# Performance work log

Measured on AMD Instinct MI355X. Metric: run time of the kernel, lower is better.

Reference implementation:

```python
import jax, jax.numpy as jnp
import numpy as np

IN_FEATURES = 1024
OUT_FEATURES = 1024
NUM_GMM = 5
MAX_STD = 3.0
ROWS = (IN_FEATURES + 1) * OUT_FEATURES  # (in+1)*out rows of GMM params


def setup_inputs() -> dict:
    key = jax.random.key(0)
    kx, km, kl, kw = jax.random.split(key, 4)
    x = jax.random.normal(kx, (4096, IN_FEATURES), dtype=jnp.float32)
    mean = jax.random.normal(km, (ROWS, NUM_GMM), dtype=jnp.float32)
    logstd = jax.random.normal(kl, (ROWS, NUM_GMM), dtype=jnp.float32)
    weight = jax.random.normal(kw, (ROWS, NUM_GMM), dtype=jnp.float32)
    return {"x": x, "mean": mean, "logstd": logstd, "weight": weight}


def reference(x, mean, logstd, weight):
    # GMM weight sampling: Categorical(softmax(weight)) picks a component per row,
    # then Normal(mean_sel, exp(tanh(logstd_sel)*max_std)) is sampled.
    key = jax.random.key(42)
    kcat, knorm = jax.random.split(key)
    # categorical with logits == Categorical(probs=softmax(weight))
    idx = jax.random.categorical(kcat, weight, axis=-1)  # [ROWS] int
    sel_mean = jnp.take_along_axis(mean, idx[:, None], axis=1)[:, 0]      # [ROWS]
    sel_logstd = jnp.take_along_axis(logstd, idx[:, None], axis=1)[:, 0]  # [ROWS]
    sel_std = jnp.exp(jnp.tanh(sel_logstd) * MAX_STD)
    eps = jax.random.normal(knorm, (mean.shape[0],), dtype=mean.dtype)
    weight_bias = sel_mean + sel_std * eps  # torch .sample() -> no grad flow
    weight_bias = jax.lax.stop_gradient(weight_bias)
    bias = weight_bias[:OUT_FEATURES]                                   # [out]
    W = weight_bias[OUT_FEATURES:].reshape(OUT_FEATURES, IN_FEATURES)   # [out, in]
    return x @ W.T + bias
```

## Files before the change

kernel.cpp:

```cpp
#include <hip/hip_runtime.h>
#include <cstdint>
#include <cmath>

#define IN_FEATURES 1024
#define OUT_FEATURES 1024
#define NUM_GMM 5
#define ROWS ((IN_FEATURES + 1) * OUT_FEATURES)

struct U2 { uint32_t a, b; };

__host__ __device__ constexpr uint32_t rotl32c(uint32_t x, int d) {
  return (x << d) | (x >> (32 - d));
}

#define TF_ROUND(r) { x0 += x1; x1 = rotl32c(x1, (r)); x1 ^= x0; }
__host__ __device__ constexpr U2 threefry2x32(uint32_t k0, uint32_t k1,
                                              uint32_t x0, uint32_t x1) {
  const uint32_t ks0 = k0, ks1 = k1, ks2 = k0 ^ k1 ^ 0x1BD11BDAu;
  x0 += ks0; x1 += ks1;
  TF_ROUND(13) TF_ROUND(15) TF_ROUND(26) TF_ROUND(6)
  x0 += ks1; x1 += ks2 + 1u;
  TF_ROUND(17) TF_ROUND(29) TF_ROUND(16) TF_ROUND(24)
  x0 += ks2; x1 += ks0 + 2u;
  TF_ROUND(13) TF_ROUND(15) TF_ROUND(26) TF_ROUND(6)
  x0 += ks0; x1 += ks1 + 3u;
  TF_ROUND(17) TF_ROUND(29) TF_ROUND(16) TF_ROUND(24)
  x0 += ks1; x1 += ks2 + 4u;
  TF_ROUND(13) TF_ROUND(15) TF_ROUND(26) TF_ROUND(6)
  x0 += ks2; x1 += ks0 + 5u;
  return U2{x0, x1};
}

constexpr U2 KC = threefry2x32(0u, 42u, 0u, 0u);
constexpr U2 KN = threefry2x32(0u, 42u, 0u, 1u);
constexpr uint32_t KCAT0  = KC.a;
constexpr uint32_t KCAT1  = KC.b;
constexpr uint32_t KNORM0 = KN.a;
constexpr uint32_t KNORM1 = KN.b;

__device__ inline float u01_from_bits(uint32_t bits) {
  return __uint_as_float((bits >> 9) | 0x3F800000u) - 1.0f;
}

__device__ inline float log_f32_acc(float x) {
  uint32_t ix = __float_as_uint(x);
  int e = (int)(ix >> 23) - 127;
  float mf = __uint_as_float((ix & 0x007FFFFFu) | 0x3F800000u);
  if (mf > 1.4142135381698608f) { mf *= 0.5f; e += 1; }
  double m = (double)mf;
  double d = m + 1.0;
  double r = (double)__builtin_amdgcn_rcpf((float)d);
  r = r * (2.0 - d * r);
  r = r * (2.0 - d * r);
  double t = (m - 1.0) * r;
  double t2 = t * t;
  double p = 1.0 / 15.0;
  p = fma(p, t2, 1.0 / 13.0);
  p = fma(p, t2, 1.0 / 11.0);
  p = fma(p, t2, 1.0 / 9.0);
  p = fma(p, t2, 1.0 / 7.0);
  p = fma(p, t2, 1.0 / 5.0);
  p = fma(p, t2, 1.0 / 3.0);
  p = fma(p, t2, 1.0);
  double res = fma((double)e, 0.693147180559945309417, 2.0 * t * p);
  return (float)res;
}

__device__ inline float u_from_bits_clamped(uint32_t bits) {
  float f = u01_from_bits(bits);
  return fmaxf(1.17549435e-38f, f + 1.17549435e-38f);
}

__device__ inline float gumbel_acc(uint32_t bits) {
  float u = u_from_bits_clamped(bits);
  float t1 = log_f32_acc(u);
  float t2 = log_f32_acc(-t1);
  return -t2;
}

__device__ inline float gumbel_fast(uint32_t bits) {
  float u = u_from_bits_clamped(bits);
  float t1 = __logf(u);
  return -__logf(-t1);
}

__device__ inline float erfinv_xla(float x) {
  float s = (1.0f - x) * (1.0f + x);
  float w = -__logf(s);
  float p;
  if (w < 5.0f) {
    w = w - 2.5f;
    p = 2.81022636e-08f;
    p = fmaf(p, w, 3.43273939e-07f);
    p = fmaf(p, w, -3.5233877e-06f);
    p = fmaf(p, w, -4.39150654e-06f);
    p = fmaf(p, w, 0.00021858087f);
    p = fmaf(p, w, -0.00125372503f);
    p = fmaf(p, w, -0.00417768164f);
    p = fmaf(p, w, 0.246640727f);
    p = fmaf(p, w, 1.50140941f);
  } else {
    w = sqrtf(w) - 3.0f;
    p = -0.000200214257f;
    p = fmaf(p, w, 0.000100950558f);
    p = fmaf(p, w, 0.00134934322f);
    p = fmaf(p, w, -0.00367342844f);
    p = fmaf(p, w, 0.00573950773f);
    p = fmaf(p, w, -0.0076224613f);
    p = fmaf(p, w, 0.00943887047f);
    p = fmaf(p, w, 1.00167406f);
    p = fmaf(p, w, 2.83297682f);
  }
  return p * x;
}

__device__ inline float normal_from_bits(uint32_t bits) {
  float f = u01_from_bits(bits);
  const float lo = -0.99999994f;
  float u = fmaxf(lo, f * 2.0f + lo);
  return 1.4142135623730951f * erfinv_xla(u);
}

__device__ inline unsigned short f32_to_bf16_rne(float f) {
  uint32_t u = __float_as_uint(f);
  return (unsigned short)((u + 0x7FFFu + ((u >> 16) & 1u)) >> 16);
}

__global__ __launch_bounds__(256) void prep_kernel(
    const float* __restrict__ mean, const float* __restrict__ logstd,
    const float* __restrict__ weight, const float* __restrict__ x,
    unsigned short* __restrict__ wh, float* __restrict__ bias_f32,
    unsigned short* __restrict__ xh, int n_chunks) {
  const int r = blockIdx.x * 256 + threadIdx.x;

  const float* wrow = weight + (size_t)r * NUM_GMM;
  const float* mrow = mean   + (size_t)r * NUM_GMM;
  const float* lrow = logstd + (size_t)r * NUM_GMM;
  float wv[NUM_GMM], mv[NUM_GMM], lv[NUM_GMM];
#pragma unroll
  for (int g = 0; g < NUM_GMM; ++g) {
    wv[g] = wrow[g];
    mv[g] = mrow[g];
    lv[g] = lrow[g];
  }

  if (r < n_chunks) {
    int i = r * 8;
    float4 a = *(const float4*)(x + i);
    float4 b = *(const float4*)(x + i + 4);
    union { unsigned short s[8]; uint4 v; } o;
    o.s[0] = f32_to_bf16_rne(a.x); o.s[1] = f32_to_bf16_rne(a.y);
    o.s[2] = f32_to_bf16_rne(a.z); o.s[3] = f32_to_bf16_rne(a.w);
    o.s[4] = f32_to_bf16_rne(b.x); o.s[5] = f32_to_bf16_rne(b.y);
    o.s[6] = f32_to_bf16_rne(b.z); o.s[7] = f32_to_bf16_rne(b.w);
    *(uint4*)(xh + i) = o.v;
  }

  uint32_t bits[NUM_GMM];
  float v[NUM_GMM];
#pragma unroll
  for (int g = 0; g < NUM_GMM; ++g) {
    U2 t = threefry2x32(KCAT0, KCAT1, 0u, (uint32_t)(r * NUM_GMM + g));
    bits[g] = t.a ^ t.b;
    v[g] = gumbel_fast(bits[g]) + wv[g];
  }
  int idx = 0;
  float best = v[0], second = -3.402823466e+38f;
#pragma unroll
  for (int g = 1; g < NUM_GMM; ++g) {
    if (v[g] > best) { second = best; best = v[g]; idx = g; }
    else if (v[g] > second) { second = v[g]; }
  }
  if (__builtin_expect(best - second < 1e-3f, 0)) {
    idx = 0;
    best = -3.402823466e+38f;
#pragma unroll
    for (int g = 0; g < NUM_GMM; ++g) {
      float va = gumbel_acc(bits[g]) + wv[g];
      if (va > best) { best = va; idx = g; }
    }
  }

  U2 tn = threefry2x32(KNORM0, KNORM1, 0u, (uint32_t)r);
  float eps = normal_from_bits(tn.a ^ tn.b);

  float m = mv[0], l = lv[0];
#pragma unroll
  for (int g = 1; g < NUM_GMM; ++g) {
    bool sel = (idx == g);
    m = sel ? mv[g] : m;
    l = sel ? lv[g] : l;
  }
  float e2 = __expf(2.0f * l);
  float th = 1.0f - 2.0f * __builtin_amdgcn_rcpf(e2 + 1.0f);
  float sd = __expf(3.0f * th);
  float wbv = m + sd * eps;
  wh[r] = f32_to_bf16_rne(wbv);
  if (r < OUT_FEATURES) bias_f32[r] = wbv;
}

typedef __attribute__((ext_vector_type(8))) short bf16x8;
typedef __attribute__((ext_vector_type(4))) float f32x4;

#define GBM 128
#define GBN 128
#define GBK 64

__device__ inline void load_lds16(const void* g, void* l) {
  __builtin_amdgcn_global_load_lds(
      (const __attribute__((address_space(1))) unsigned int*)g,
      (__attribute__((address_space(3))) unsigned int*)l, 16, 0, 0);
}

__global__ __launch_bounds__(256) void gemm_mfma_kernel(
    const unsigned short* __restrict__ xh, const unsigned short* __restrict__ wh,
    const float* __restrict__ bias, float* __restrict__ out) {
  __shared__ unsigned short As[3][GBM * GBK];
  __shared__ unsigned short Bs[3][GBN * GBK];

  const unsigned short* W = wh + OUT_FEATURES;
  const int tid = threadIdx.x;
  const int w = tid >> 6;
  const int L = tid & 63;
  const int wr = w >> 1;
  const int wc = w & 1;

  const int lin = blockIdx.x;
  const int xcd = lin & 7;
  const int loc = lin >> 3;
  const int m_tile = ((xcd >> 1) * 8 + (loc >> 2)) * GBM;
  const int n_tile = ((xcd & 1) * 4 + (loc & 3)) * GBN;

  const int sm = tid & 15;
  const int sh = (tid >> 4) & 3;
  const int sk = (tid >> 6) & 1;
  const int sb = tid >> 7;
  const int kofs = sk * 32 + sh * 8;

  const unsigned short* gA[4];
  const unsigned short* gB[4];
#pragma unroll
  for (int i = 0; i < 4; ++i)
    gA[i] = xh + (size_t)(m_tile + (2 * i + sb) * 16 + sm) * IN_FEATURES + kofs;
#pragma unroll
  for (int i = 0; i < 4; ++i)
    gB[i] = W + (size_t)(n_tile + (2 * i + sb) * 16 + sm) * IN_FEATURES + kofs;

  f32x4 acc[4][4];
#pragma unroll
  for (int a = 0; a < 4; ++a)
#pragma unroll
    for (int b = 0; b < 4; ++b) acc[a][b] = (f32x4){0.f, 0.f, 0.f, 0.f};

#define STAGE(buf, k0)                                                    \
  {                                                                       \
    _Pragma("unroll")                                                     \
    for (int i = 0; i < 4; ++i)                                           \
      load_lds16(gA[i] + (k0), &As[buf][(size_t)(tid + 256 * i) * 8]);    \
    _Pragma("unroll")                                                     \
    for (int i = 0; i < 4; ++i)                                           \
      load_lds16(gB[i] + (k0), &Bs[buf][(size_t)(tid + 256 * i) * 8]);    \
  }

  STAGE(0, 0)
  STAGE(1, GBK)

  const int NK = IN_FEATURES / GBK;
#pragma unroll
  for (int kt = 0; kt < NK; ++kt) {
    if (kt < NK - 1) {
      asm volatile("s_waitcnt vmcnt(8)" ::: "memory");
    } else {
      asm volatile("s_waitcnt vmcnt(0)" ::: "memory");
    }
    asm volatile("s_barrier" ::: "memory");
    if (kt + 2 < NK) STAGE((kt + 2) % 3, (kt + 2) * GBK)
    const unsigned short* Ab = As[kt % 3];
    const unsigned short* Bb = Bs[kt % 3];
#pragma unroll
    for (int s = 0; s < 2; ++s) {
      bf16x8 a[4], b[4];
#pragma unroll
      for (int m = 0; m < 4; ++m)
        a[m] = *(const bf16x8*)(Ab + (((wr * 4 + m) * 2 + s) * 64 + L) * 8);
#pragma unroll
      for (int n = 0; n < 4; ++n)
        b[n] = *(const bf16x8*)(Bb + (((wc * 4 + n) * 2 + s) * 64 + L) * 8);
#pragma unroll
      for (int m = 0; m < 4; ++m)
#pragma unroll
        for (int n = 0; n < 4; ++n)
          acc[m][n] = __builtin_amdgcn_mfma_f32_16x16x32_bf16(
              a[m], b[n], acc[m][n], 0, 0, 0);
    }
  }

  const int colL = L & 15;
  const int rowq = (L >> 4) * 4;
  float bv[4];
#pragma unroll
  for (int nb = 0; nb < 4; ++nb)
    bv[nb] = bias[n_tile + wc * 64 + nb * 16 + colL];
#pragma unroll
  for (int mb = 0; mb < 4; ++mb) {
#pragma unroll
    for (int reg = 0; reg < 4; ++reg) {
      int row = m_tile + wr * 64 + mb * 16 + rowq + reg;
#pragma unroll
      for (int nb = 0; nb < 4; ++nb) {
        out[(size_t)row * OUT_FEATURES + n_tile + wc * 64 + nb * 16 + colL] =
            acc[mb][nb][reg] + bv[nb];
      }
    }
  }
}

extern "C" void kernel_launch(void* const* d_in, const int* in_sizes, int n_in,
                              void* d_out, int out_size, void* d_ws, size_t ws_size,
                              hipStream_t stream) {
  const float* x      = (const float*)d_in[0];
  const float* mean   = (const float*)d_in[1];
  const float* logstd = (const float*)d_in[2];
  const float* weight = (const float*)d_in[3];
  float* out = (float*)d_out;

  const int M = in_sizes[0] / IN_FEATURES;

  unsigned short* xh = (unsigned short*)d_ws;
  unsigned short* wh = (unsigned short*)((char*)d_ws + (size_t)M * IN_FEATURES * 2);
  float* biasf = (float*)((char*)wh + (size_t)ROWS * 2);

  const int n_chunks = M * IN_FEATURES / 8;
  prep_kernel<<<ROWS / 256, 256, 0, stream>>>(
      mean, logstd, weight, x, wh, biasf, xh, n_chunks);

  dim3 grid((OUT_FEATURES / GBN) * (M / GBM));
  gemm_mfma_kernel<<<grid, 256, 0, stream>>>(xh, wh, biasf, out);
}
```

Before: 133.9 us.

## Fuse prep and GEMM into one cooperative kernel with grid sync

Replaces the two launches (sampling/conversion prep, then bf16 MFMA GEMM) with a single cooperative kernel of 256 blocks of 512 threads. Each thread first grid-strides over the x-to-bf16 conversion and the GMM row sampling, with software-pipelined loads of the next row's parameters, then hits a grid-wide barrier before the GEMM. The GEMM now splits K across two wave groups per tile and reduces their partial sums through LDS before the bias add and store. This removes the second launch and the tail gap between kernels, but the sampling phase runs with fewer threads and has to pay for a grid sync. If the cooperative launch fails it falls back to the two-kernel path.

```diff
diff --git a/kernel.cpp b/kernel.cpp
--- a/kernel.cpp
+++ b/kernel.cpp
@@ -1,4 +1,5 @@
 #include <hip/hip_runtime.h>
+#include <hip/hip_cooperative_groups.h>
 #include <cstdint>
 #include <cmath>
 
@@ -126,90 +127,254 @@
   return (unsigned short)((u + 0x7FFFu + ((u >> 16) & 1u)) >> 16);
 }
 
+__device__ inline void load_row5(const float* __restrict__ weight,
+                                 const float* __restrict__ mean,
+                                 const float* __restrict__ logstd, int r,
+                                 float wv[NUM_GMM], float mv[NUM_GMM],
+                                 float lv[NUM_GMM]) {
+#pragma unroll
+  for (int g = 0; g < NUM_GMM; ++g) {
+    wv[g] = weight[(size_t)r * NUM_GMM + g];
+    mv[g] = mean[(size_t)r * NUM_GMM + g];
+    lv[g] = logstd[(size_t)r * NUM_GMM + g];
+  }
+}
+
+__device__ inline void sample_row(int r, const float wv[NUM_GMM],
+                                  const float mv[NUM_GMM],
+                                  const float lv[NUM_GMM],
+                                  unsigned short* __restrict__ wh,
+                                  float* __restrict__ bias_f32) {
+  uint32_t bits[NUM_GMM];
+  float v[NUM_GMM];
+#pragma unroll
+  for (int g = 0; g < NUM_GMM; ++g) {
+    U2 t = threefry2x32(KCAT0, KCAT1, 0u, (uint32_t)(r * NUM_GMM + g));
+    bits[g] = t.a ^ t.b;
+    v[g] = gumbel_fast(bits[g]) + wv[g];
+  }
+  int idx = 0;
+  float best = v[0], second = -3.402823466e+38f;
+#pragma unroll
+  for (int g = 1; g < NUM_GMM; ++g) {
+    if (v[g] > best) { second = best; best = v[g]; idx = g; }
+    else if (v[g] > second) { second = v[g]; }
+  }
+  if (__builtin_expect(best - second < 1e-3f, 0)) {
+    idx = 0;
+    best = -3.402823466e+38f;
+#pragma unroll
+    for (int g = 0; g < NUM_GMM; ++g) {
+      float va = gumbel_acc(bits[g]) + wv[g];
+      if (va > best) { best = va; idx = g; }
+    }
+  }
+
+  U2 tn = threefry2x32(KNORM0, KNORM1, 0u, (uint32_t)r);
+  float eps = normal_from_bits(tn.a ^ tn.b);
+
+  float m = mv[0], l = lv[0];
+#pragma unroll
+  for (int g = 1; g < NUM_GMM; ++g) {
+    bool sel = (idx == g);
+    m = sel ? mv[g] : m;
+    l = sel ? lv[g] : l;
+  }
+  float e2 = __expf(2.0f * l);
+  float th = 1.0f - 2.0f * __builtin_amdgcn_rcpf(e2 + 1.0f);
+  float sd = __expf(3.0f * th);
+  float wbv = m + sd * eps;
+  wh[r] = f32_to_bf16_rne(wbv);
+  if (r < OUT_FEATURES) bias_f32[r] = wbv;
+}
+
+__device__ inline void convert_chunk(const float* __restrict__ x,
+                                     unsigned short* __restrict__ xh, int c) {
+  int i = c * 8;
+  float4 a = *(const float4*)(x + i);
+  float4 b = *(const float4*)(x + i + 4);
+  union { unsigned short s[8]; uint4 v; } o;
+  o.s[0] = f32_to_bf16_rne(a.x); o.s[1] = f32_to_bf16_rne(a.y);
+  o.s[2] = f32_to_bf16_rne(a.z); o.s[3] = f32_to_bf16_rne(a.w);
+  o.s[4] = f32_to_bf16_rne(b.x); o.s[5] = f32_to_bf16_rne(b.y);
+  o.s[6] = f32_to_bf16_rne(b.z); o.s[7] = f32_to_bf16_rne(b.w);
+  *(uint4*)(xh + i) = o.v;
+}
+
+typedef __attribute__((ext_vector_type(8))) short bf16x8;
+typedef __attribute__((ext_vector_type(4))) float f32x4;
+
+#define GBM 128
+#define GBN 128
+#define GBK 64
+
+__device__ inline void load_lds16(const void* g, void* l) {
+  __builtin_amdgcn_global_load_lds(
+      (const __attribute__((address_space(1))) unsigned int*)g,
+      (__attribute__((address_space(3))) unsigned int*)l, 16, 0, 0);
+}
+
+__global__ __launch_bounds__(512, 2) void fused_kernel(
+    const float* __restrict__ mean, const float* __restrict__ logstd,
+    const float* __restrict__ weight, const float* __restrict__ x,
+    unsigned short* __restrict__ wh, float* __restrict__ bias_f32,
+    unsigned short* __restrict__ xh, float* __restrict__ out, int n_chunks) {
+  __shared__ __align__(16) unsigned short smem[3 * 16384];
+  const int tid = threadIdx.x;
+  const int gt = blockIdx.x * 512 + tid;
+
+  for (int c = gt; c < n_chunks; c += 131072) convert_chunk(x, xh, c);
+
+  {
+    float wA[NUM_GMM], mA[NUM_GMM], lA[NUM_GMM];
+    float wB[NUM_GMM], mB[NUM_GMM], lB[NUM_GMM];
+    load_row5(weight, mean, logstd, gt, wA, mA, lA);
+#pragma unroll 1
+    for (int j = 0; j < 8; j += 2) {
+      int r0 = gt + 131072 * j;
+      int r1 = r0 + 131072;
+      load_row5(weight, mean, logstd, r1, wB, mB, lB);
+      sample_row(r0, wA, mA, lA, wh, bias_f32);
+      if (j + 2 < 8)
+        load_row5(weight, mean, logstd, r1 + 131072, wA, mA, lA);
+      sample_row(r1, wB, mB, lB, wh, bias_f32);
+    }
+    if (gt < ROWS - 131072 * 8) {
+      int r = 131072 * 8 + gt;
+      load_row5(weight, mean, logstd, r, wA, mA, lA);
+      sample_row(r, wA, mA, lA, wh, bias_f32);
+    }
+  }
+
+  __threadfence();
+  cooperative_groups::this_grid().sync();
+
+  const unsigned short* W = wh + OUT_FEATURES;
+  const int w = tid >> 6;
+  const int L = tid & 63;
+  const int s  = w >> 2;
+  const int wr = (w >> 1) & 1;
+  const int wc = w & 1;
+
+  const int lin = blockIdx.x;
+  const int xcd = lin & 7;
+  const int loc = lin >> 3;
+  const int m_tile = ((xcd >> 1) * 8 + (loc >> 2)) * GBM;
+  const int n_tile = ((xcd & 1) * 4 + (loc & 3)) * GBN;
+
+  const int sm = tid & 15;
+  const int sh = (tid >> 4) & 3;
+  const int sk = (tid >> 6) & 1;
+  const int sb = tid >> 7;
+  const int kofs = sk * 32 + sh * 8;
+
+  const unsigned short* gA[2];
+  const unsigned short* gB[2];
+#pragma unroll
+  for (int i = 0; i < 2; ++i) {
+    gA[i] = xh + (size_t)(m_tile + (4 * i + sb) * 16 + sm) * IN_FEATURES + kofs;
+    gB[i] = W + (size_t)(n_tile + (4 * i + sb) * 16 + sm) * IN_FEATURES + kofs;
+  }
+
+  f32x4 acc[4][4];
+#pragma unroll
+  for (int a = 0; a < 4; ++a)
+#pragma unroll
+    for (int b = 0; b < 4; ++b) acc[a][b] = (f32x4){0.f, 0.f, 0.f, 0.f};
+
+#define ABASE(buf) (smem + (buf) * 16384)
+#define BBASE(buf) (smem + (buf) * 16384 + 8192)
+#define FSTAGE(buf, k0)                                                      \
+  {                                                                          \
+    _Pragma("unroll")                                                        \
+    for (int i = 0; i < 2; ++i)                                              \
+      load_lds16(gA[i] + (k0), ABASE(buf) + (size_t)(tid + 512 * i) * 8);    \
+    _Pragma("unroll")                                                        \
+    for (int i = 0; i < 2; ++i)                                              \
+      load_lds16(gB[i] + (k0), BBASE(buf) + (size_t)(tid + 512 * i) * 8);    \
+  }
+
+  FSTAGE(0, 0)
+  FSTAGE(1, GBK)
+
+  const int NK = IN_FEATURES / GBK;
+#pragma unroll
+  for (int kt = 0; kt < NK; ++kt) {
+    if (kt < NK - 1) {
+      asm volatile("s_waitcnt vmcnt(4)" ::: "memory");
+    } else {
+      asm volatile("s_waitcnt vmcnt(0)" ::: "memory");
+    }
+    asm volatile("s_barrier" ::: "memory");
+    if (kt + 2 < NK) FSTAGE((kt + 2) % 3, (kt + 2) * GBK)
+    const unsigned short* Ab = ABASE(kt % 3);
+    const unsigned short* Bb = BBASE(kt % 3);
+    bf16x8 a[4], b[4];
+#pragma unroll
+    for (int m = 0; m < 4; ++m)
+      a[m] = *(const bf16x8*)(Ab + (((wr * 4 + m) * 2 + s) * 64 + L) * 8);
+#pragma unroll
+    for (int n = 0; n < 4; ++n)
+      b[n] = *(const bf16x8*)(Bb + (((wc * 4 + n) * 2 + s) * 64 + L) * 8);
+#pragma unroll
+    for (int m = 0; m < 4; ++m)
+#pragma unroll
+      for (int n = 0; n < 4; ++n)
+        acc[m][n] = __builtin_amdgcn_mfma_f32_16x16x32_bf16(
+            a[m], b[n], acc[m][n], 0, 0, 0);
+  }
+
+  __syncthreads();
+  float* sc = (float*)smem;
+  if (w >= 4) {
+    const int q = w & 3;
+#pragma unroll
+    for (int m = 0; m < 4; ++m)
+#pragma unroll
+      for (int n = 0; n < 4; ++n)
+        *(f32x4*)(sc + q * 4096 + ((m * 4 + n) * 64 + L) * 4) = acc[m][n];
+  }
+  __syncthreads();
+  if (w < 4) {
+    const int q = w & 3;
+#pragma unroll
+    for (int m = 0; m < 4; ++m)
+#pragma unroll
+      for (int n = 0; n < 4; ++n) {
+        f32x4 o = *(const f32x4*)(sc + q * 4096 + ((m * 4 + n) * 64 + L) * 4);
+        acc[m][n] += o;
+      }
+    const int colL = L & 15;
+    const int rowq = (L >> 4) * 4;
+    float bv[4];
+#pragma unroll
+    for (int nb = 0; nb < 4; ++nb)
+      bv[nb] = bias_f32[n_tile + wc * 64 + nb * 16 + colL];
+#pragma unroll
+    for (int mb = 0; mb < 4; ++mb) {
+#pragma unroll
+      for (int reg = 0; reg < 4; ++reg) {
+        int row = m_tile + wr * 64 + mb * 16 + rowq + reg;
+#pragma unroll
+        for (int nb = 0; nb < 4; ++nb) {
+          out[(size_t)row * OUT_FEATURES + n_tile + wc * 64 + nb * 16 + colL] =
+              acc[mb][nb][reg] + bv[nb];
+        }
+      }
+    }
+  }
+}
+
 __global__ __launch_bounds__(256) void prep_kernel(
     const float* __restrict__ mean, const float* __restrict__ logstd,
     const float* __restrict__ weight, const float* __restrict__ x,
     unsigned short* __restrict__ wh, float* __restrict__ bias_f32,
     unsigned short* __restrict__ xh, int n_chunks) {
   const int r = blockIdx.x * 256 + threadIdx.x;
-
-  const float* wrow = weight + (size_t)r * NUM_GMM;
-  const float* mrow = mean   + (size_t)r * NUM_GMM;
-  const float* lrow = logstd + (size_t)r * NUM_GMM;
   float wv[NUM_GMM], mv[NUM_GMM], lv[NUM_GMM];
-#pragma unroll
-  for (int g = 0; g < NUM_GMM; ++g) {
-    wv[g] = wrow[g];
-    mv[g] = mrow[g];
-    lv[g] = lrow[g];
-  }
-
-  if (r < n_chunks) {
-    int i = r * 8;
-    float4 a = *(const float4*)(x + i);
-    float4 b = *(const float4*)(x + i + 4);
-    union { unsigned short s[8]; uint4 v; } o;
-    o.s[0] = f32_to_bf16_rne(a.x); o.s[1] = f32_to_bf16_rne(a.y);
-    o.s[2] = f32_to_bf16_rne(a.z); o.s[3] = f32_to_bf16_rne(a.w);
-    o.s[4] = f32_to_bf16_rne(b.x); o.s[5] = f32_to_bf16_rne(b.y);
-    o.s[6] = f32_to_bf16_rne(b.z); o.s[7] = f32_to_bf16_rne(b.w);
-    *(uint4*)(xh + i) = o.v;
-  }
-
-  uint32_t bits[NUM_GMM];
-  float v[NUM_GMM];
-#pragma unroll
-  for (int g = 0; g < NUM_GMM; ++g) {
-    U2 t = threefry2x32(KCAT0, KCAT1, 0u, (uint32_t)(r * NUM_GMM + g));
-    bits[g] = t.a ^ t.b;
-    v[g] = gumbel_fast(bits[g]) + wv[g];
-  }
-  int idx = 0;
-  float best = v[0], second = -3.402823466e+38f;
-#pragma unroll
-  for (int g = 1; g < NUM_GMM; ++g) {
-    if (v[g] > best) { second = best; best = v[g]; idx = g; }
-    else if (v[g] > second) { second = v[g]; }
-  }
-  if (__builtin_expect(best - second < 1e-3f, 0)) {
-    idx = 0;
-    best = -3.402823466e+38f;
-#pragma unroll
-    for (int g = 0; g < NUM_GMM; ++g) {
-      float va = gumbel_acc(bits[g]) + wv[g];
-      if (va > best) { best = va; idx = g; }
-    }
-  }
-
-  U2 tn = threefry2x32(KNORM0, KNORM1, 0u, (uint32_t)r);
-  float eps = normal_from_bits(tn.a ^ tn.b);
-
-  float m = mv[0], l = lv[0];
-#pragma unroll
-  for (int g = 1; g < NUM_GMM; ++g) {
-    bool sel = (idx == g);
-    m = sel ? mv[g] : m;
-    l = sel ? lv[g] : l;
-  }
-  float e2 = __expf(2.0f * l);
-  float th = 1.0f - 2.0f * __builtin_amdgcn_rcpf(e2 + 1.0f);
-  float sd = __expf(3.0f * th);
-  float wbv = m + sd * eps;
-  wh[r] = f32_to_bf16_rne(wbv);
-  if (r < OUT_FEATURES) bias_f32[r] = wbv;
-}
-
-typedef __attribute__((ext_vector_type(8))) short bf16x8;
-typedef __attribute__((ext_vector_type(4))) float f32x4;
-
-#define GBM 128
-#define GBN 128
-#define GBK 64
-
-__device__ inline void load_lds16(const void* g, void* l) {
-  __builtin_amdgcn_global_load_lds(
-      (const __attribute__((address_space(1))) unsigned int*)g,
-      (__attribute__((address_space(3))) unsigned int*)l, 16, 0, 0);
+  load_row5(weight, mean, logstd, r, wv, mv, lv);
+  if (r < n_chunks) convert_chunk(x, xh, r);
+  sample_row(r, wv, mv, lv, wh, bias_f32);
 }
 
 __global__ __launch_bounds__(256) void gemm_mfma_kernel(
@@ -330,10 +495,17 @@
   unsigned short* wh = (unsigned short*)((char*)d_ws + (size_t)M * IN_FEATURES * 2);
   float* biasf = (float*)((char*)wh + (size_t)ROWS * 2);
 
-  const int n_chunks = M * IN_FEATURES / 8;
-  prep_kernel<<<ROWS / 256, 256, 0, stream>>>(
-      mean, logstd, weight, x, wh, biasf, xh, n_chunks);
-
-  dim3 grid((OUT_FEATURES / GBN) * (M / GBM));
-  gemm_mfma_kernel<<<grid, 256, 0, stream>>>(xh, wh, biasf, out);
-}
+  int n_chunks = M * IN_FEATURES / 8;
+
+  void* args[] = {(void*)&mean, (void*)&logstd, (void*)&weight, (void*)&x,
+                  (void*)&wh, (void*)&biasf, (void*)&xh, (void*)&out,
+                  (void*)&n_chunks};
+  hipError_t e = hipLaunchCooperativeKernel((void*)fused_kernel, dim3(256),
+                                            dim3(512), args, 0, stream);
+  if (e != hipSuccess) {
+    (void)hipGetLastError();
+    prep_kernel<<<ROWS / 256, 256, 0, stream>>>(
+        mean, logstd, weight, x, wh, biasf, xh, n_chunks);
+    gemm_mfma_kernel<<<dim3(256), 256, 0, stream>>>(xh, wh, biasf, out);
+  }
+}
```

After: 227.8 us. 70.1% more time.

## Split GEMM K-halves across two wave groups with LDS reduction

Applied to the files above, without the earlier changes.

The GEMM block grows from 256 to 512 threads. The two wave groups each compute the 128x128 tile over a different 32-wide half of every 64-wide K step, and their partial accumulators are summed through LDS before the bias-add store. Each thread now issues half as many global-to-LDS loads per stage, and the per-CU wave count doubles to improve latency hiding. The cost is an extra LDS round-trip and two block barriers in the epilogue. The prep kernel is only split into helper functions.

```diff
diff --git a/kernel.cpp b/kernel.cpp
--- a/kernel.cpp
+++ b/kernel.cpp
@@ -126,77 +126,90 @@
   return (unsigned short)((u + 0x7FFFu + ((u >> 16) & 1u)) >> 16);
 }
 
+__device__ inline void load_row5(const float* __restrict__ weight,
+                                 const float* __restrict__ mean,
+                                 const float* __restrict__ logstd, int r,
+                                 float wv[NUM_GMM], float mv[NUM_GMM],
+                                 float lv[NUM_GMM]) {
+#pragma unroll
+  for (int g = 0; g < NUM_GMM; ++g) {
+    wv[g] = weight[(size_t)r * NUM_GMM + g];
+    mv[g] = mean[(size_t)r * NUM_GMM + g];
+    lv[g] = logstd[(size_t)r * NUM_GMM + g];
+  }
+}
+
+__device__ inline void sample_row(int r, const float wv[NUM_GMM],
+                                  const float mv[NUM_GMM],
+                                  const float lv[NUM_GMM],
+                                  unsigned short* __restrict__ wh,
+                                  float* __restrict__ bias_f32) {
+  uint32_t bits[NUM_GMM];
+  float v[NUM_GMM];
+#pragma unroll
+  for (int g = 0; g < NUM_GMM; ++g) {
+    U2 t = threefry2x32(KCAT0, KCAT1, 0u, (uint32_t)(r * NUM_GMM + g));
+    bits[g] = t.a ^ t.b;
+    v[g] = gumbel_fast(bits[g]) + wv[g];
+  }
+  int idx = 0;
+  float best = v[0], second = -3.402823466e+38f;
+#pragma unroll
+  for (int g = 1; g < NUM_GMM; ++g) {
+    if (v[g] > best) { second = best; best = v[g]; idx = g; }
+    else if (v[g] > second) { second = v[g]; }
+  }
+  if (__builtin_expect(best - second < 1e-3f, 0)) {
+    idx = 0;
+    best = -3.402823466e+38f;
+#pragma unroll
+    for (int g = 0; g < NUM_GMM; ++g) {
+      float va = gumbel_acc(bits[g]) + wv[g];
+      if (va > best) { best = va; idx = g; }
+    }
+  }
+
+  U2 tn = threefry2x32(KNORM0, KNORM1, 0u, (uint32_t)r);
+  float eps = normal_from_bits(tn.a ^ tn.b);
+
+  float m = mv[0], l = lv[0];
+#pragma unroll
+  for (int g = 1; g < NUM_GMM; ++g) {
+    bool sel = (idx == g);
+    m = sel ? mv[g] : m;
+    l = sel ? lv[g] : l;
+  }
+  float e2 = __expf(2.0f * l);
+  float th = 1.0f - 2.0f * __builtin_amdgcn_rcpf(e2 + 1.0f);
+  float sd = __expf(3.0f * th);
+  float wbv = m + sd * eps;
+  wh[r] = f32_to_bf16_rne(wbv);
+  if (r < OUT_FEATURES) bias_f32[r] = wbv;
+}
+
+__device__ inline void convert_chunk(const float* __restrict__ x,
+                                     unsigned short* __restrict__ xh, int c) {
+  int i = c * 8;
+  float4 a = *(const float4*)(x + i);
+  float4 b = *(const float4*)(x + i + 4);
+  union { unsigned short s[8]; uint4 v; } o;
+  o.s[0] = f32_to_bf16_rne(a.x); o.s[1] = f32_to_bf16_rne(a.y);
+  o.s[2] = f32_to_bf16_rne(a.z); o.s[3] = f32_to_bf16_rne(a.w);
+  o.s[4] = f32_to_bf16_rne(b.x); o.s[5] = f32_to_bf16_rne(b.y);
+  o.s[6] = f32_to_bf16_rne(b.z); o.s[7] = f32_to_bf16_rne(b.w);
+  *(uint4*)(xh + i) = o.v;
+}
+
 __global__ __launch_bounds__(256) void prep_kernel(
     const float* __restrict__ mean, const float* __restrict__ logstd,
     const float* __restrict__ weight, const float* __restrict__ x,
     unsigned short* __restrict__ wh, float* __restrict__ bias_f32,
     unsigned short* __restrict__ xh, int n_chunks) {
   const int r = blockIdx.x * 256 + threadIdx.x;
-
-  const float* wrow = weight + (size_t)r * NUM_GMM;
-  const float* mrow = mean   + (size_t)r * NUM_GMM;
-  const float* lrow = logstd + (size_t)r * NUM_GMM;
   float wv[NUM_GMM], mv[NUM_GMM], lv[NUM_GMM];
-#pragma unroll
-  for (int g = 0; g < NUM_GMM; ++g) {
-    wv[g] = wrow[g];
-    mv[g] = mrow[g];
-    lv[g] = lrow[g];
-  }
-
-  if (r < n_chunks) {
-    int i = r * 8;
-    float4 a = *(const float4*)(x + i);
-    float4 b = *(const float4*)(x + i + 4);
-    union { unsigned short s[8]; uint4 v; } o;
-    o.s[0] = f32_to_bf16_rne(a.x); o.s[1] = f32_to_bf16_rne(a.y);
-    o.s[2] = f32_to_bf16_rne(a.z); o.s[3] = f32_to_bf16_rne(a.w);
-    o.s[4] = f32_to_bf16_rne(b.x); o.s[5] = f32_to_bf16_rne(b.y);
-    o.s[6] = f32_to_bf16_rne(b.z); o.s[7] = f32_to_bf16_rne(b.w);
-    *(uint4*)(xh + i) = o.v;
-  }
-
-  uint32_t bits[NUM_GMM];
-  float v[NUM_GMM];
-#pragma unroll
-  for (int g = 0; g < NUM_GMM; ++g) {
-    U2 t = threefry2x32(KCAT0, KCAT1, 0u, (uint32_t)(r * NUM_GMM + g));
-    bits[g] = t.a ^ t.b;
-    v[g] = gumbel_fast(bits[g]) + wv[g];
-  }
-  int idx = 0;
-  float best = v[0], second = -3.402823466e+38f;
-#pragma unroll
-  for (int g = 1; g < NUM_GMM; ++g) {
-    if (v[g] > best) { second = best; best = v[g]; idx = g; }
-    else if (v[g] > second) { second = v[g]; }
-  }
-  if (__builtin_expect(best - second < 1e-3f, 0)) {
-    idx = 0;
-    best = -3.402823466e+38f;
-#pragma unroll
-    for (int g = 0; g < NUM_GMM; ++g) {
-      float va = gumbel_acc(bits[g]) + wv[g];
-      if (va > best) { best = va; idx = g; }
-    }
-  }
-
-  U2 tn = threefry2x32(KNORM0, KNORM1, 0u, (uint32_t)r);
-  float eps = normal_from_bits(tn.a ^ tn.b);
-
-  float m = mv[0], l = lv[0];
-#pragma unroll
-  for (int g = 1; g < NUM_GMM; ++g) {
-    bool sel = (idx == g);
-    m = sel ? mv[g] : m;
-    l = sel ? lv[g] : l;
-  }
-  float e2 = __expf(2.0f * l);
-  float th = 1.0f - 2.0f * __builtin_amdgcn_rcpf(e2 + 1.0f);
-  float sd = __expf(3.0f * th);
-  float wbv = m + sd * eps;
-  wh[r] = f32_to_bf16_rne(wbv);
-  if (r < OUT_FEATURES) bias_f32[r] = wbv;
+  load_row5(weight, mean, logstd, r, wv, mv, lv);
+  if (r < n_chunks) convert_chunk(x, xh, r);
+  sample_row(r, wv, mv, lv, wh, bias_f32);
 }
 
 typedef __attribute__((ext_vector_type(8))) short bf16x8;
@@ -212,17 +225,17 @@
       (__attribute__((address_space(3))) unsigned int*)l, 16, 0, 0);
 }
 
-__global__ __launch_bounds__(256) void gemm_mfma_kernel(
+__global__ __launch_bounds__(512) void gemm_mfma_kernel(
     const unsigned short* __restrict__ xh, const unsigned short* __restrict__ wh,
     const float* __restrict__ bias, float* __restrict__ out) {
-  __shared__ unsigned short As[3][GBM * GBK];
-  __shared__ unsigned short Bs[3][GBN * GBK];
+  __shared__ __align__(16) unsigned short smem[3 * 16384];
 
   const unsigned short* W = wh + OUT_FEATURES;
   const int tid = threadIdx.x;
   const int w = tid >> 6;
   const int L = tid & 63;
-  const int wr = w >> 1;
+  const int s  = w >> 2;
+  const int wr = (w >> 1) & 1;
   const int wc = w & 1;
 
   const int lin = blockIdx.x;
@@ -237,14 +250,13 @@
   const int sb = tid >> 7;
   const int kofs = sk * 32 + sh * 8;
 
-  const unsigned short* gA[4];
-  const unsigned short* gB[4];
-#pragma unroll
-  for (int i = 0; i < 4; ++i)
-    gA[i] = xh + (size_t)(m_tile + (2 * i + sb) * 16 + sm) * IN_FEATURES + kofs;
-#pragma unroll
-  for (int i = 0; i < 4; ++i)
-    gB[i] = W + (size_t)(n_tile + (2 * i + sb) * 16 + sm) * IN_FEATURES + kofs;
+  const unsigned short* gA[2];
+  const unsigned short* gB[2];
+#pragma unroll
+  for (int i = 0; i < 2; ++i) {
+    gA[i] = xh + (size_t)(m_tile + (4 * i + sb) * 16 + sm) * IN_FEATURES + kofs;
+    gB[i] = W + (size_t)(n_tile + (4 * i + sb) * 16 + sm) * IN_FEATURES + kofs;
+  }
 
   f32x4 acc[4][4];
 #pragma unroll
@@ -252,64 +264,84 @@
 #pragma unroll
     for (int b = 0; b < 4; ++b) acc[a][b] = (f32x4){0.f, 0.f, 0.f, 0.f};
 
-#define STAGE(buf, k0)                                                    \
-  {                                                                       \
-    _Pragma("unroll")                                                     \
-    for (int i = 0; i < 4; ++i)                                           \
-      load_lds16(gA[i] + (k0), &As[buf][(size_t)(tid + 256 * i) * 8]);    \
-    _Pragma("unroll")                                                     \
-    for (int i = 0; i < 4; ++i)                                           \
-      load_lds16(gB[i] + (k0), &Bs[buf][(size_t)(tid + 256 * i) * 8]);    \
-  }
-
-  STAGE(0, 0)
-  STAGE(1, GBK)
+#define ABASE(buf) (smem + (buf) * 16384)
+#define BBASE(buf) (smem + (buf) * 16384 + 8192)
+#define FSTAGE(buf, k0)                                                      \
+  {                                                                          \
+    _Pragma("unroll")                                                        \
+    for (int i = 0; i < 2; ++i)                                              \
+      load_lds16(gA[i] + (k0), ABASE(buf) + (size_t)(tid + 512 * i) * 8);    \
+    _Pragma("unroll")                                                        \
+    for (int i = 0; i < 2; ++i)                                              \
+      load_lds16(gB[i] + (k0), BBASE(buf) + (size_t)(tid + 512 * i) * 8);    \
+  }
+
+  FSTAGE(0, 0)
+  FSTAGE(1, GBK)
 
   const int NK = IN_FEATURES / GBK;
 #pragma unroll
   for (int kt = 0; kt < NK; ++kt) {
     if (kt < NK - 1) {
-      asm volatile("s_waitcnt vmcnt(8)" ::: "memory");
+      asm volatile("s_waitcnt vmcnt(4)" ::: "memory");
     } else {
       asm volatile("s_waitcnt vmcnt(0)" ::: "memory");
     }
     asm volatile("s_barrier" ::: "memory");
-    if (kt + 2 < NK) STAGE((kt + 2) % 3, (kt + 2) * GBK)
-    const unsigned short* Ab = As[kt % 3];
-    const unsigned short* Bb = Bs[kt % 3];
-#pragma unroll
-    for (int s = 0; s < 2; ++s) {
-      bf16x8 a[4], b[4];
-#pragma unroll
-      for (int m = 0; m < 4; ++m)
-        a[m] = *(const bf16x8*)(Ab + (((wr * 4 + m) * 2 + s) * 64 + L) * 8);
+    if (kt + 2 < NK) FSTAGE((kt + 2) % 3, (kt + 2) * GBK)
+    const unsigned short* Ab = ABASE(kt % 3);
+    const unsigned short* Bb = BBASE(kt % 3);
+    bf16x8 a[4], b[4];
+#pragma unroll
+    for (int m = 0; m < 4; ++m)
+      a[m] = *(const bf16x8*)(Ab + (((wr * 4 + m) * 2 + s) * 64 + L) * 8);
+#pragma unroll
+    for (int n = 0; n < 4; ++n)
+      b[n] = *(const bf16x8*)(Bb + (((wc * 4 + n) * 2 + s) * 64 + L) * 8);
+#pragma unroll
+    for (int m = 0; m < 4; ++m)
 #pragma unroll
       for (int n = 0; n < 4; ++n)
-        b[n] = *(const bf16x8*)(Bb + (((wc * 4 + n) * 2 + s) * 64 + L) * 8);
-#pragma unroll
-      for (int m = 0; m < 4; ++m)
-#pragma unroll
-        for (int n = 0; n < 4; ++n)
-          acc[m][n] = __builtin_amdgcn_mfma_f32_16x16x32_bf16(
-              a[m], b[n], acc[m][n], 0, 0, 0);
-    }
-  }
-
-  const int colL = L & 15;
-  const int rowq = (L >> 4) * 4;
-  float bv[4];
-#pragma unroll
-  for (int nb = 0; nb < 4; ++nb)
-    bv[nb] = bias[n_tile + wc * 64 + nb * 16 + colL];
-#pragma unroll
-  for (int mb = 0; mb < 4; ++mb) {
-#pragma unroll
-    for (int reg = 0; reg < 4; ++reg) {
-      int row = m_tile + wr * 64 + mb * 16 + rowq + reg;
-#pragma unroll
-      for (int nb = 0; nb < 4; ++nb) {
-        out[(size_t)row * OUT_FEATURES + n_tile + wc * 64 + nb * 16 + colL] =
-            acc[mb][nb][reg] + bv[nb];
+        acc[m][n] = __builtin_amdgcn_mfma_f32_16x16x32_bf16(
+            a[m], b[n], acc[m][n], 0, 0, 0);
+  }
+
+  __syncthreads();
+  float* sc = (float*)smem;
+  if (w >= 4) {
+    const int q = w & 3;
+#pragma unroll
+    for (int m = 0; m < 4; ++m)
+#pragma unroll
+      for (int n = 0; n < 4; ++n)
+        *(f32x4*)(sc + q * 4096 + ((m * 4 + n) * 64 + L) * 4) = acc[m][n];
+  }
+  __syncthreads();
+  if (w < 4) {
+    const int q = w & 3;
+#pragma unroll
+    for (int m = 0; m < 4; ++m)
+#pragma unroll
+      for (int n = 0; n < 4; ++n) {
+        f32x4 o = *(const f32x4*)(sc + q * 4096 + ((m * 4 + n) * 64 + L) * 4);
+        acc[m][n] += o;
+      }
+    const int colL = L & 15;
+    const int rowq = (L >> 4) * 4;
+    float bv[4];
+#pragma unroll
+    for (int nb = 0; nb < 4; ++nb)
+      bv[nb] = bias[n_tile + wc * 64 + nb * 16 + colL];
+#pragma unroll
+    for (int mb = 0; mb < 4; ++mb) {
+#pragma unroll
+      for (int reg = 0; reg < 4; ++reg) {
+        int row = m_tile + wr * 64 + mb * 16 + rowq + reg;
+#pragma unroll
+        for (int nb = 0; nb < 4; ++nb) {
+          out[(size_t)row * OUT_FEATURES + n_tile + wc * 64 + nb * 16 + colL] =
+              acc[mb][nb][reg] + bv[nb];
+        }
       }
     }
   }
@@ -334,6 +366,5 @@
   prep_kernel<<<ROWS / 256, 256, 0, stream>>>(
       mean, logstd, weight, x, wh, biasf, xh, n_chunks);
 
-  dim3 grid((OUT_FEATURES / GBN) * (M / GBM));
-  gemm_mfma_kernel<<<grid, 256, 0, stream>>>(xh, wh, biasf, out);
-}
+  gemm_mfma_kernel<<<dim3(256), 512, 0, stream>>>(xh, wh, biasf, out);
+}
```

Measured after the change: 132.0 us. Within noise of the previous version (-1.5%).
